# Performance work log

Hardware: AMD Instinct MI355X
Metric: run time of the kernel (lower is better)

Reference implementation:

```python
import jax, jax.numpy as jnp
import numpy as np

SIZE = (2, 2)  # max-unpooling kernel size from init_kwargs


def setup_inputs() -> dict:
    key = jax.random.key(0)
    k1, k2 = jax.random.split(key)
    B, H, W, C = 16, 64, 64, 256
    Ho, Wo = H * SIZE[0], W * SIZE[1]
    updates = jax.random.normal(k1, (B, H, W, C), dtype=jnp.float32)
    # mask holds flat argmax indices into the per-batch output volume [Ho, Wo, C]
    mask = jax.random.randint(k2, (B, H, W, C), 0, Ho * Wo * C, dtype=jnp.int32)
    return {"updates": updates, "mask": mask}


def reference(updates, mask):
    B, H, W, C = updates.shape
    Ho, Wo = H * SIZE[0], W * SIZE[1]
    mask = mask.astype(jnp.int32)
    # Decode flat indices into (y, x); feature index comes from the channel position.
    y = mask // (Wo * C)                      # [B,H,W,C]
    x = (mask // C) % Wo                      # [B,H,W,C]
    b = jnp.arange(B, dtype=jnp.int32).reshape(B, 1, 1, 1)   # broadcasts
    f = jnp.arange(C, dtype=jnp.int32)                        # broadcasts
    out = jnp.zeros((B, Ho, Wo, C), dtype=updates.dtype)
    # tf.scatter_nd sums duplicate indices -> use .add for faithfulness
    return out.at[b, y, x, f].add(updates)
```

## Files before the change

### kernel.cpp

```cpp
#include <hip/hip_runtime.h>


using u32 = unsigned int;
using u16 = unsigned short;
using u8  = unsigned char;
typedef float f32x4 __attribute__((ext_vector_type(4)));
typedef u32   u32x4 __attribute__((ext_vector_type(4)));

constexpr int kB   = 16;
constexpr int kC   = 256;
constexpr int kHW  = 4096;
constexpr long kNin  = (long)kB * kHW * kC;
constexpr long kNout = (long)kB * 16384 * kC;
constexpr int kBkt  = 256;
constexpr int kCap  = 5120;
constexpr int kE    = 8192;
constexpr int kPad  = kE + 3 * kBkt;
constexpr int kGrp  = kPad / 4;

__device__ inline u32 f2h(float x) { return (u32)__builtin_bit_cast(u16, (_Float16)x); }
__device__ inline float h2f(u32 b) { return (float)__builtin_bit_cast(_Float16, (u16)(b & 0xFFFFu)); }

__global__ __launch_bounds__(512) void bucket_kernel(
        const int4*   __restrict__ mask,
        const float4* __restrict__ upd,
        u32* __restrict__ g_cursor,
        u32* __restrict__ g_pay) {
    __shared__ u32 counts[kBkt];
    __shared__ u32 packed[kBkt];
    __shared__ u32 wsum[4];
    __shared__ u32 s_tot;
    __shared__ u32 lds_pay[kPad];
    __shared__ u32 lds_dstg[kGrp];
    int tid = threadIdx.x, blk = blockIdx.x;
    int b   = blk >> 7;
    if (tid < kBkt) counts[tid] = 0;
    {
        u32x4* z4 = (u32x4*)lds_pay;
        u32x4 z = (u32x4){0u, 0u, 0u, 0u};
#pragma unroll
        for (int i = 0; i < 5; ++i) {
            int g = tid + 512 * i;
            if (g < kGrp) z4[g] = z;
        }
    }
    __syncthreads();

    u32 pay[16], bs[16];
#pragma unroll
    for (int k = 0; k < 4; ++k) {
        int v4 = blk * 2048 + k * 512 + tid;
        int4   m = mask[v4];
        float4 u = upd[v4];
        int c0 = (v4 * 4) & 255;
        int p; u32 bkt, slot;
        p = m.x >> 8; bkt = (u32)(p >> 6); slot = atomicAdd(&counts[bkt], 1u);
        pay[4*k+0] = ((u32)(p & 63) << 24) | ((u32)(c0 + 0) << 16) | f2h(u.x);
        bs [4*k+0] = (bkt << 16) | slot;
        p = m.y >> 8; bkt = (u32)(p >> 6); slot = atomicAdd(&counts[bkt], 1u);
        pay[4*k+1] = ((u32)(p & 63) << 24) | ((u32)(c0 + 1) << 16) | f2h(u.y);
        bs [4*k+1] = (bkt << 16) | slot;
        p = m.z >> 8; bkt = (u32)(p >> 6); slot = atomicAdd(&counts[bkt], 1u);
        pay[4*k+2] = ((u32)(p & 63) << 24) | ((u32)(c0 + 2) << 16) | f2h(u.z);
        bs [4*k+2] = (bkt << 16) | slot;
        p = m.w >> 8; bkt = (u32)(p >> 6); slot = atomicAdd(&counts[bkt], 1u);
        pay[4*k+3] = ((u32)(p & 63) << 24) | ((u32)(c0 + 3) << 16) | f2h(u.w);
        bs [4*k+3] = (bkt << 16) | slot;
    }
    __syncthreads();

    if (tid < kBkt) {
        u32 cnt  = counts[tid];
        u32 cntp = (cnt + 3u) & ~3u;
        u32 gb   = atomicAdd(&g_cursor[(b << 8) + tid], cntp);
        u32 x = cntp;
#pragma unroll
        for (int s = 1; s < 64; s <<= 1) {
            u32 v = __shfl_up(x, s, 64);
            if ((tid & 63) >= s) x += v;
        }
        int w = tid >> 6;
        if ((tid & 63) == 63) wsum[w] = x;
        __syncthreads();
        u32 excl = x - cntp;
        u32 s0 = wsum[0], s1 = wsum[1], s2 = wsum[2];
        if (w > 0) excl += s0;
        if (w > 1) excl += s1;
        if (w > 2) excl += s2;
        gb = min(gb, (u32)kCap);
        packed[tid] = (gb << 16) | excl;
        if (tid == 255) s_tot = excl + cntp;
    } else {
        __syncthreads();
    }
    __syncthreads();

    u32 breg = (u32)(b << 8) * (u32)kCap;
#pragma unroll
    for (int k = 0; k < 16; ++k) {
        u32 bkt = bs[k] >> 16, slot = bs[k] & 0xFFFFu;
        u32 pk  = packed[bkt];
        u32 pos = (pk & 0xFFFFu) + slot;
        lds_pay[pos] = pay[k];
        if ((slot & 3u) == 0u) {
            u32 gslot = (pk >> 16) + slot;
            lds_dstg[pos >> 2] = (gslot < (u32)kCap)
                ? (breg + bkt * (u32)kCap + gslot)
                : 0xFFFFFFFFu;
        }
    }
    __syncthreads();

    u32 ng = s_tot >> 2;
    const u32x4* lp4 = (const u32x4*)lds_pay;
    for (u32 g = tid; g < ng; g += 512) {
        u32 d   = lds_dstg[g];
        u32x4 v = lp4[g];
        if (d != 0xFFFFFFFFu)
            *(u32x4*)(g_pay + d) = v;
    }
}

__global__ __launch_bounds__(1024) void expand_kernel(
        const u32* __restrict__ g_cursor,
        const u32* __restrict__ g_pay,
        f32x4*     __restrict__ out) {
    __shared__ float bins[64 * kC];
    __shared__ u32 s_n;
    int tid = threadIdx.x, blk = blockIdx.x;
    f32x4* b4 = (f32x4*)bins;
    f32x4 z = (f32x4){0.f, 0.f, 0.f, 0.f};
#pragma unroll
    for (int i = 0; i < 4; ++i) b4[tid + 1024 * i] = z;
    if (tid == 0) s_n = min(g_cursor[blk], (u32)kCap);
    __syncthreads();
    u32 n = s_n;
    const u32*   payp = g_pay + (size_t)blk * kCap;
    const uint4* pay4 = (const uint4*)payp;
    u32 n4 = n >> 2;
    for (u32 i = tid; i < n4; i += 1024) {
        uint4 p = pay4[i];
        if (p.x) atomicAdd(&bins[(p.x >> 24) * kC + ((p.x >> 16) & 0xFFu)], h2f(p.x));
        if (p.y) atomicAdd(&bins[(p.y >> 24) * kC + ((p.y >> 16) & 0xFFu)], h2f(p.y));
        if (p.z) atomicAdd(&bins[(p.z >> 24) * kC + ((p.z >> 16) & 0xFFu)], h2f(p.z));
        if (p.w) atomicAdd(&bins[(p.w >> 24) * kC + ((p.w >> 16) & 0xFFu)], h2f(p.w));
    }
    __syncthreads();
#pragma unroll
    for (int i = 0; i < 4; ++i)
        __builtin_nontemporal_store(b4[tid + 1024 * i],
                                    &out[(size_t)blk * 4096 + tid + 1024 * i]);
}

__global__ __launch_bounds__(256) void zero_kernel(float4* __restrict__ out) {
    int i = blockIdx.x * 256 + threadIdx.x;
    out[i] = make_float4(0.f, 0.f, 0.f, 0.f);
}
__global__ __launch_bounds__(256) void scatter_kernel(
        const float4* __restrict__ upd,
        const int4*  __restrict__ mask,
        float*       __restrict__ out) {
    int i = blockIdx.x * 256 + threadIdx.x;
    int4  m = mask[i];
    float4 u = upd[i];
    int base_idx = i << 2;
    int b = base_idx >> 20;
    int c = base_idx & (kC - 1);
    int obase = b << 22;
    atomicAdd(out + (obase | (m.x & ~0xFF) | (c + 0)), u.x);
    atomicAdd(out + (obase | (m.y & ~0xFF) | (c + 1)), u.y);
    atomicAdd(out + (obase | (m.z & ~0xFF) | (c + 2)), u.z);
    atomicAdd(out + (obase | (m.w & ~0xFF) | (c + 3)), u.w);
}

extern "C" void kernel_launch(void* const* d_in, const int* in_sizes, int n_in,
                              void* d_out, int out_size, void* d_ws, size_t ws_size,
                              hipStream_t stream) {
    const float* updates = (const float*)d_in[0];
    const int*   mask    = (const int*)d_in[1];
    float*       out     = (float*)d_out;

    const size_t cursor_bytes = (size_t)kB * kBkt * 4;
    const size_t pay_off      = 1 << 16;
    const size_t need = pay_off + (size_t)kB * kBkt * kCap * 4;
    if (ws_size >= need) {
        u32* g_cursor = (u32*)d_ws;
        u32* g_pay    = (u32*)((char*)d_ws + pay_off);
        (void)hipMemsetAsync(g_cursor, 0, cursor_bytes, stream);
        bucket_kernel<<<kB * 128, 512, 0, stream>>>(
            (const int4*)mask, (const float4*)updates, g_cursor, g_pay);
        expand_kernel<<<kB * kBkt, 1024, 0, stream>>>(
            g_cursor, g_pay, (f32x4*)out);
    } else {
        zero_kernel<<<kNout / 4 / 256, 256, 0, stream>>>((float4*)out);
        scatter_kernel<<<kNin / 4 / 256, 256, 0, stream>>>(
            (const float4*)updates, (const int4*)mask, out);
    }
}
```

Baseline: 431.4 us.

## Fuse memset, bucket and expand passes into one cooperative persistent kernel

Replaces the memset plus two-kernel pipeline with a single cooperative-launch persistent kernel. It clears the cursors, buckets the input chunks, then runs the expand pass, using grid-wide syncs between phases and a shared 64KB LDS buffer for both phases. This removes the launch gaps between kernels, at the cost of grid syncs and a persistent grid that may run at lower occupancy (512 threads, occupancy-limited grid) during expand. The old path is kept as a fallback if the cooperative launch fails.

```diff
diff --git a/kernel.cpp b/kernel.cpp
--- a/kernel.cpp
+++ b/kernel.cpp
@@ -1,25 +1,169 @@
 #include <hip/hip_runtime.h>
-
+#include <hip/hip_cooperative_groups.h>
+
+
+namespace cg = cooperative_groups;
 
 using u32 = unsigned int;
 using u16 = unsigned short;
-using u8  = unsigned char;
 typedef float f32x4 __attribute__((ext_vector_type(4)));
 typedef u32   u32x4 __attribute__((ext_vector_type(4)));
 
 constexpr int kB   = 16;
 constexpr int kC   = 256;
-constexpr int kHW  = 4096;
-constexpr long kNin  = (long)kB * kHW * kC;
-constexpr long kNout = (long)kB * 16384 * kC;
+constexpr long kNin  = 16777216L;
+constexpr long kNout = 67108864L;
 constexpr int kBkt  = 256;
 constexpr int kCap  = 5120;
 constexpr int kE    = 8192;
+constexpr int kChunks = kB * (4096 * kC / kE / kC) * 128 / 128;
 constexpr int kPad  = kE + 3 * kBkt;
 constexpr int kGrp  = kPad / 4;
+constexpr int kNBkts = kB * kBkt;
+constexpr int PAY = 0, DSTG = 8960, CNT = 11200, PKD = 11456;
 
 __device__ inline u32 f2h(float x) { return (u32)__builtin_bit_cast(u16, (_Float16)x); }
 __device__ inline float h2f(u32 b) { return (float)__builtin_bit_cast(_Float16, (u16)(b & 0xFFFFu)); }
+
+__global__ __launch_bounds__(512, 4) void fused_kernel(
+        const int4*   __restrict__ mask,
+        const float4* __restrict__ upd,
+        u32* __restrict__ g_cursor,
+        u32* __restrict__ g_pay,
+        f32x4* __restrict__ out) {
+    __shared__ u32 lds[16384];
+    __shared__ u32 wsum[4];
+    __shared__ u32 s_tot;
+    cg::grid_group grid = cg::this_grid();
+    int tid = threadIdx.x, blk = blockIdx.x, nblk = gridDim.x;
+
+    for (int i = blk * 512 + tid; i < kNBkts; i += nblk * 512)
+        atomicExch(&g_cursor[i], 0u);
+    __threadfence();
+    grid.sync();
+
+    u32* counts = lds + CNT;
+    u32* packed = lds + PKD;
+    u32* pay_s  = lds + PAY;
+    u32* dstg   = lds + DSTG;
+    for (int chunk = blk; chunk < 2048; chunk += nblk) {
+        int b = chunk >> 7;
+        if (tid < kBkt) counts[tid] = 0;
+        {
+            u32x4* z4 = (u32x4*)pay_s;
+            u32x4 z = (u32x4){0u, 0u, 0u, 0u};
+#pragma unroll
+            for (int i = 0; i < 5; ++i) {
+                int g = tid + 512 * i;
+                if (g < kGrp) z4[g] = z;
+            }
+        }
+        __syncthreads();
+
+        u32 pay[16], bs[16];
+#pragma unroll
+        for (int k = 0; k < 4; ++k) {
+            int v4 = chunk * 2048 + k * 512 + tid;
+            int4   m = mask[v4];
+            float4 u = upd[v4];
+            int c0 = (v4 * 4) & 255;
+            int p; u32 bkt, slot;
+            p = m.x >> 8; bkt = (u32)(p >> 6); slot = atomicAdd(&counts[bkt], 1u);
+            pay[4*k+0] = ((u32)(p & 63) << 24) | ((u32)(c0 + 0) << 16) | f2h(u.x);
+            bs [4*k+0] = (bkt << 16) | slot;
+            p = m.y >> 8; bkt = (u32)(p >> 6); slot = atomicAdd(&counts[bkt], 1u);
+            pay[4*k+1] = ((u32)(p & 63) << 24) | ((u32)(c0 + 1) << 16) | f2h(u.y);
+            bs [4*k+1] = (bkt << 16) | slot;
+            p = m.z >> 8; bkt = (u32)(p >> 6); slot = atomicAdd(&counts[bkt], 1u);
+            pay[4*k+2] = ((u32)(p & 63) << 24) | ((u32)(c0 + 2) << 16) | f2h(u.z);
+            bs [4*k+2] = (bkt << 16) | slot;
+            p = m.w >> 8; bkt = (u32)(p >> 6); slot = atomicAdd(&counts[bkt], 1u);
+            pay[4*k+3] = ((u32)(p & 63) << 24) | ((u32)(c0 + 3) << 16) | f2h(u.w);
+            bs [4*k+3] = (bkt << 16) | slot;
+        }
+        __syncthreads();
+
+        if (tid < kBkt) {
+            u32 cnt  = counts[tid];
+            u32 cntp = (cnt + 3u) & ~3u;
+            u32 gb   = atomicAdd(&g_cursor[(b << 8) + tid], cntp);
+            u32 x = cntp;
+#pragma unroll
+            for (int s = 1; s < 64; s <<= 1) {
+                u32 v = __shfl_up(x, s, 64);
+                if ((tid & 63) >= s) x += v;
+            }
+            int w = tid >> 6;
+            if ((tid & 63) == 63) wsum[w] = x;
+            __syncthreads();
+            u32 excl = x - cntp;
+            u32 s0 = wsum[0], s1 = wsum[1], s2 = wsum[2];
+            if (w > 0) excl += s0;
+            if (w > 1) excl += s1;
+            if (w > 2) excl += s2;
+            gb = min(gb, (u32)kCap);
+            packed[tid] = (gb << 16) | excl;
+            if (tid == 255) s_tot = excl + cntp;
+        } else {
+            __syncthreads();
+        }
+        __syncthreads();
+
+        u32 breg = (u32)(b << 8) * (u32)kCap;
+#pragma unroll
+        for (int k = 0; k < 16; ++k) {
+            u32 bkt = bs[k] >> 16, slot = bs[k] & 0xFFFFu;
+            u32 pk  = packed[bkt];
+            u32 pos = (pk & 0xFFFFu) + slot;
+            pay_s[pos] = pay[k];
+            if ((slot & 3u) == 0u) {
+                u32 gslot = (pk >> 16) + slot;
+                dstg[pos >> 2] = (gslot < (u32)kCap)
+                    ? (breg + bkt * (u32)kCap + gslot)
+                    : 0xFFFFFFFFu;
+            }
+        }
+        __syncthreads();
+
+        u32 ng = s_tot >> 2;
+        const u32x4* lp4 = (const u32x4*)pay_s;
+        for (u32 g = tid; g < ng; g += 512) {
+            u32 d   = dstg[g];
+            u32x4 v = lp4[g];
+            if (d != 0xFFFFFFFFu)
+                *(u32x4*)(g_pay + d) = v;
+        }
+        __syncthreads();
+    }
+
+    __threadfence();
+    grid.sync();
+
+    f32x4* b4   = (f32x4*)lds;
+    float* bins = (float*)lds;
+    for (int bkt = blk; bkt < kNBkts; bkt += nblk) {
+        f32x4 z = (f32x4){0.f, 0.f, 0.f, 0.f};
+#pragma unroll
+        for (int i = 0; i < 8; ++i) b4[tid + 512 * i] = z;
+        u32 n = min(g_cursor[bkt], (u32)kCap);
+        __syncthreads();
+        const uint4* pay4 = (const uint4*)(g_pay + (size_t)bkt * kCap);
+        u32 n4 = n >> 2;
+        for (u32 i = tid; i < n4; i += 512) {
+            uint4 p = pay4[i];
+            if (p.x) atomicAdd(&bins[(p.x >> 24) * kC + ((p.x >> 16) & 0xFFu)], h2f(p.x));
+            if (p.y) atomicAdd(&bins[(p.y >> 24) * kC + ((p.y >> 16) & 0xFFu)], h2f(p.y));
+            if (p.z) atomicAdd(&bins[(p.z >> 24) * kC + ((p.z >> 16) & 0xFFu)], h2f(p.z));
+            if (p.w) atomicAdd(&bins[(p.w >> 24) * kC + ((p.w >> 16) & 0xFFu)], h2f(p.w));
+        }
+        __syncthreads();
+#pragma unroll
+        for (int i = 0; i < 8; ++i)
+            __builtin_nontemporal_store(b4[tid + 512 * i],
+                                        &out[(size_t)bkt * 4096 + tid + 512 * i]);
+        __syncthreads();
+    }
+}
 
 __global__ __launch_bounds__(512) void bucket_kernel(
         const int4*   __restrict__ mask,
@@ -45,7 +189,6 @@
         }
     }
     __syncthreads();
-
     u32 pay[16], bs[16];
 #pragma unroll
     for (int k = 0; k < 4; ++k) {
@@ -68,7 +211,6 @@
         bs [4*k+3] = (bkt << 16) | slot;
     }
     __syncthreads();
-
     if (tid < kBkt) {
         u32 cnt  = counts[tid];
         u32 cntp = (cnt + 3u) & ~3u;
@@ -94,7 +236,6 @@
         __syncthreads();
     }
     __syncthreads();
-
     u32 breg = (u32)(b << 8) * (u32)kCap;
 #pragma unroll
     for (int k = 0; k < 16; ++k) {
@@ -110,7 +251,6 @@
         }
     }
     __syncthreads();
-
     u32 ng = s_tot >> 2;
     const u32x4* lp4 = (const u32x4*)lds_pay;
     for (u32 g = tid; g < ng; g += 512) {
@@ -135,8 +275,7 @@
     if (tid == 0) s_n = min(g_cursor[blk], (u32)kCap);
     __syncthreads();
     u32 n = s_n;
-    const u32*   payp = g_pay + (size_t)blk * kCap;
-    const uint4* pay4 = (const uint4*)payp;
+    const uint4* pay4 = (const uint4*)(g_pay + (size_t)blk * kCap);
     u32 n4 = n >> 2;
     for (u32 i = tid; i < n4; i += 1024) {
         uint4 p = pay4[i];
@@ -180,16 +319,37 @@
     const int*   mask    = (const int*)d_in[1];
     float*       out     = (float*)d_out;
 
-    const size_t cursor_bytes = (size_t)kB * kBkt * 4;
+    const size_t cursor_bytes = (size_t)kNBkts * 4;
     const size_t pay_off      = 1 << 16;
-    const size_t need = pay_off + (size_t)kB * kBkt * kCap * 4;
+    const size_t need = pay_off + (size_t)kNBkts * kCap * 4;
     if (ws_size >= need) {
         u32* g_cursor = (u32*)d_ws;
         u32* g_pay    = (u32*)((char*)d_ws + pay_off);
+
+        static int coop_nb = -1;
+        if (coop_nb < 0) {
+            int nb = 0;
+            if (hipOccupancyMaxActiveBlocksPerMultiprocessor(
+                    &nb, fused_kernel, 512, 0) != hipSuccess) nb = 0;
+            coop_nb = nb;
+        }
+        if (coop_nb > 0) {
+            int grid = coop_nb * 256;
+            if (grid > 2048) grid = 2048;
+            const int4*   m4 = (const int4*)mask;
+            const float4* u4 = (const float4*)updates;
+            f32x4*        o4 = (f32x4*)out;
+            void* args[] = {(void*)&m4, (void*)&u4, (void*)&g_cursor,
+                            (void*)&g_pay, (void*)&o4};
+            if (hipLaunchCooperativeKernel((void*)fused_kernel, dim3(grid),
+                                           dim3(512), args, 0, stream)
+                    == hipSuccess)
+                return;
+        }
         (void)hipMemsetAsync(g_cursor, 0, cursor_bytes, stream);
         bucket_kernel<<<kB * 128, 512, 0, stream>>>(
             (const int4*)mask, (const float4*)updates, g_cursor, g_pay);
-        expand_kernel<<<kB * kBkt, 1024, 0, stream>>>(
+        expand_kernel<<<kNBkts, 1024, 0, stream>>>(
             g_cursor, g_pay, (f32x4*)out);
     } else {
         zero_kernel<<<kNout / 4 / 256, 256, 0, stream>>>((float4*)out);
```

Result: slower. 583.8 us (+35.3%).
